# Kernel tuning notes

Hardware: AMD Instinct MI355X
Metric: run time of the kernel (lower is better)

## Reference

```python
import jax, jax.numpy as jnp
import numpy as np


def _fps_one_batch(pts, num_samples):
    """Furthest point sampling for one batch segment.
    pts: [Npb, 3]. Seeds with point 0 (pointops furthestsampling convention).
    Returns int32 indices [num_samples].
    """
    # initial min-distance to the seed point
    dist = jnp.sum((pts - pts[0]) ** 2, axis=-1)  # [Npb]

    def step(dist, _):
        idx = jnp.argmax(dist)                      # furthest remaining point
        d = jnp.sum((pts - pts[idx]) ** 2, axis=-1)  # dist to new sample
        return jnp.minimum(dist, d), idx.astype(jnp.int32)

    _, idxs = jax.lax.scan(step, dist, None, length=num_samples - 1)
    return jnp.concatenate([jnp.zeros((1,), jnp.int32), idxs])


def setup_inputs() -> dict:
    key = jax.random.key(0)
    N, B = 262144, 2
    Npb = N // B
    xyz = jax.random.normal(key, (N, 3), dtype=jnp.float32) * 20.0  # lidar-scale coords
    b = jnp.repeat(jnp.arange(B, dtype=jnp.float32), Npb)[:, None]
    point_bxyz = jnp.concatenate([b, xyz], axis=1)  # [N, 4] (b, x, y, z)
    return {"point_bxyz": point_bxyz, "stride": 32, "batch_size": B}


def reference(point_bxyz, stride, batch_size):
    N = point_bxyz.shape[0]
    Npb = N // batch_size                      # equal-size batch segments
    M = (Npb + stride - 1) // stride           # samples per batch (ceil)
    xyz = point_bxyz[:, 1:4].reshape(batch_size, Npb, 3)

    idx = jax.vmap(lambda p: _fps_one_batch(p, M))(xyz)          # [B, M] local indices
    gidx = idx + (jnp.arange(batch_size, dtype=jnp.int32) * Npb)[:, None]
    new_bxyz = point_bxyz[gidx.reshape(-1)]    # [B*M, 4] sampled points
    return new_bxyz
```

## Files before the change

kernel.cpp:

```cpp
#include <hip/hip_runtime.h>


#define NB    32
#define TPB   256
#define PPT   16
#define NPB   131072
#define MSAMP 4096
#define RING  2
#define KW    8
#define NWAVE 128
#define NQUAD (NWAVE * 16)
#define RB_U32 (NQUAD * 4)
#define NCAND (NWAVE * KW)
#define JCAP  64

typedef unsigned long long u64;
typedef unsigned int u32;
typedef __attribute__((ext_vector_type(4))) u32 u32x4;

__device__ __forceinline__ void st16_sys(u32* p, u32x4 v) {
  asm volatile("global_store_dwordx4 %0, %1, off sc0 sc1"
               :: "v"(p), "v"(v) : "memory");
}
__device__ __forceinline__ void ld16x8_sys(
    const u32* p0, const u32* p1, const u32* p2, const u32* p3,
    const u32* p4, const u32* p5, const u32* p6, const u32* p7,
    u32x4& q0, u32x4& q1, u32x4& q2, u32x4& q3,
    u32x4& q4, u32x4& q5, u32x4& q6, u32x4& q7) {
  asm volatile(
    "global_load_dwordx4 %0, %8, off sc0 sc1\n\t"
    "global_load_dwordx4 %1, %9, off sc0 sc1\n\t"
    "global_load_dwordx4 %2, %10, off sc0 sc1\n\t"
    "global_load_dwordx4 %3, %11, off sc0 sc1\n\t"
    "global_load_dwordx4 %4, %12, off sc0 sc1\n\t"
    "global_load_dwordx4 %5, %13, off sc0 sc1\n\t"
    "global_load_dwordx4 %6, %14, off sc0 sc1\n\t"
    "global_load_dwordx4 %7, %15, off sc0 sc1\n\t"
    "s_waitcnt vmcnt(0)"
    : "=v"(q0), "=v"(q1), "=v"(q2), "=v"(q3),
      "=v"(q4), "=v"(q5), "=v"(q6), "=v"(q7)
    : "v"(p0), "v"(p1), "v"(p2), "v"(p3),
      "v"(p4), "v"(p5), "v"(p6), "v"(p7)
    : "memory");
}

template<int CTRL>
__device__ __forceinline__ u64 dpp_move64(u64 x) {
  int lo = (int)(u32)(x & 0xFFFFFFFFull);
  int hi = (int)(u32)(x >> 32);
  int nlo = __builtin_amdgcn_update_dpp(lo, lo, CTRL, 0xF, 0xF, false);
  int nhi = __builtin_amdgcn_update_dpp(hi, hi, CTRL, 0xF, 0xF, false);
  return ((u64)(u32)nhi << 32) | (u64)(u32)nlo;
}
#define DPP_ROW_SHR(n)  (0x110 + (n))
#define DPP_BCAST15     0x142
#define DPP_BCAST31     0x143

__device__ __forceinline__ u64 dpp_max64_to63(u64 k) {
  u64 t;
  t = dpp_move64<DPP_ROW_SHR(1)>(k); if (t > k) k = t;
  t = dpp_move64<DPP_ROW_SHR(2)>(k); if (t > k) k = t;
  t = dpp_move64<DPP_ROW_SHR(4)>(k); if (t > k) k = t;
  t = dpp_move64<DPP_ROW_SHR(8)>(k); if (t > k) k = t;
  t = dpp_move64<DPP_BCAST15>(k);    if (t > k) k = t;
  t = dpp_move64<DPP_BCAST31>(k);    if (t > k) k = t;
  return k;
}
__device__ __forceinline__ u64 bcast_key(u64 k, int srclane) {
  u32 lo = (u32)__builtin_amdgcn_readlane((int)(u32)(k & 0xFFFFFFFFull), srclane);
  u32 hi = (u32)__builtin_amdgcn_readlane((int)(u32)(k >> 32), srclane);
  return ((u64)hi << 32) | (u64)lo;
}
__device__ __forceinline__ float bcast_f32(float v, int srclane) {
  return __uint_as_float((u32)__builtin_amdgcn_readlane((int)__float_as_uint(v), srclane));
}

template<int NC>
__device__ __forceinline__ int sim_wave(const u32* s_pool, int m, u32 cutd,
    int jmax, int lane, float& ox, float& oy, float& oz) {
#pragma clang fp contract(off)
  u64 ck[NC]; float cx[NC], cy[NC], cz[NC];
#pragma unroll
  for (int i = 0; i < NC; ++i) {
    int idx = lane + i * 64;
    if (idx < m) {
      const u32* b = s_pool + idx * 5;
      ck[i] = ((u64)b[1] << 32) | (u64)b[0];
      cx[i] = __uint_as_float(b[2]); cy[i] = __uint_as_float(b[3]);
      cz[i] = __uint_as_float(b[4]);
    } else { ck[i] = 0; cx[i] = cy[i] = cz[i] = 0.f; }
  }
  int j = 0;
  for (int t = 0; t < jmax; ++t) {
    u64 tk = ck[0]; float mx = cx[0], my = cy[0], mz = cz[0];
#pragma unroll
    for (int i = 1; i < NC; ++i)
      if (ck[i] > tk) { tk = ck[i]; mx = cx[i]; my = cy[i]; mz = cz[i]; }
    u64 wk = bcast_key(dpp_max64_to63(tk), 63);
    if (t > 0 && (u32)(wk >> 32) <= cutd) break;
    int wl = __ffsll(__ballot(tk == wk)) - 1;
    float wx = bcast_f32(mx, wl), wy = bcast_f32(my, wl), wz = bcast_f32(mz, wl);
    if (lane == t) { ox = wx; oy = wy; oz = wz; }
    j = t + 1;
#pragma unroll
    for (int i = 0; i < NC; ++i) {
      float dx = cx[i]-wx, dy = cy[i]-wy, dz = cz[i]-wz;
      float d2 = __fadd_rn(__fadd_rn(__fmul_rn(dx,dx), __fmul_rn(dy,dy)),
                           __fmul_rn(dz,dz));
      float nd = fminf(__uint_as_float((u32)(ck[i] >> 32)), d2);
      ck[i] = ((u64)__float_as_uint(nd) << 32) | (ck[i] & 0xFFFFFFFFull);
    }
  }
  return j;
}

__global__ __launch_bounds__(TPB, 1)
void fps_kernel(const float4* __restrict__ pts, float* __restrict__ out,
                u32* __restrict__ slots)
{
#pragma clang fp contract(off)
  const int batch = blockIdx.x >> 5;
  const int rank  = blockIdx.x & (NB - 1);
  const int tid   = threadIdx.x;
  const int lane  = tid & 63;
  const int wv    = tid >> 6;
  const int ws_id = rank * 4 + wv;

  __shared__ u32   s_quads[NWAVE * 68];
  __shared__ u32   s_pool[NCAND * 5];
  __shared__ int   s_cnt2[2];

  const float4* bpts = pts + (size_t)batch * NPB;
  u32* bslots = slots + (size_t)batch * (RING * RB_U32);
  const int base = rank * (TPB * PPT);

  float px[PPT], py[PPT], pz[PPT], dist[PPT];
  float4 seed = bpts[0];
  const float sx = seed.y, sy = seed.z, sz = seed.w;
#pragma unroll
  for (int k = 0; k < PPT; ++k) {
    float4 p = bpts[base + k * TPB + tid];
    px[k] = p.y; py[k] = p.z; pz[k] = p.w;
    float dx = px[k]-sx, dy = py[k]-sy, dz = pz[k]-sz;
    dist[k] = __fadd_rn(__fadd_rn(__fmul_rn(dx,dx), __fmul_rn(dy,dy)),
                        __fmul_rn(dz,dz));
  }
  if (rank == 0 && tid == 0) {
    float4 o; o.x=(float)batch; o.y=sx; o.z=sy; o.w=sz;
    *(float4*)(out + (size_t)batch * MSAMP * 4) = o;
  }
  if (tid == 0) { s_cnt2[0] = 0; s_cnt2[1] = 0; }
  __syncthreads();

  int S = 0; u32 r = 0;
  float ox = 0.f, oy = 0.f, oz = 0.f;

  while (S < MSAMP - 1) {
    r += 1;
    const int rem = (MSAMP - 1) - S;
    const int jmax = (rem < JCAP) ? rem : JCAP;

    u32 mask = 0; u64 tk = 0; float tx=0.f, ty=0.f, tz=0.f; int tbk = 0;
#pragma unroll
    for (int k = 0; k < PPT; ++k) {
      u64 kk = ((u64)__float_as_uint(dist[k]) << 32) | ((u64)r << 17) |
               (u64)(0x1FFFF - (base + k * TPB + tid));
      if (kk > tk) { tk = kk; tx = px[k]; ty = py[k]; tz = pz[k]; tbk = k; }
    }
    u32x4 shipq;
    for (int c = 0; c < KW; ++c) {
      u64 wk = bcast_key(dpp_max64_to63(tk), 63);
      int wl = __ffsll(__ballot(tk == wk)) - 1;
      float wx = bcast_f32(tx, wl), wy = bcast_f32(ty, wl), wz = bcast_f32(tz, wl);
      if (lane == 2*c)     { shipq.x=(u32)(wk & 0xFFFFFFFFull); shipq.y=(u32)(wk>>32);
                             shipq.z=__float_as_uint(wx); shipq.w=__float_as_uint(wy); }
      if (lane == 2*c + 1) { shipq.x=r; shipq.y=__float_as_uint(wz);
                             shipq.z=0u; shipq.w=0u; }
      if (tk == wk) {
        mask |= 1u << tbk;
        tk = 0; tx = ty = tz = 0.f; tbk = 0;
#pragma unroll
        for (int k = 0; k < PPT; ++k) {
          if (!((mask >> k) & 1u)) {
            u64 kk = ((u64)__float_as_uint(dist[k]) << 32) | ((u64)r << 17) |
                     (u64)(0x1FFFF - (base + k * TPB + tid));
            if (kk > tk) { tk = kk; tx = px[k]; ty = py[k]; tz = pz[k]; tbk = k; }
          }
        }
      }
    }

    u32* ring = bslots + (size_t)(r & (RING - 1)) * RB_U32;
    if (lane < 16) st16_sys(ring + (ws_id * 16 + lane) * 4, shipq);

    const int gb = wv * 512 + lane;
    const u32 *pp0 = ring + (gb      ) * 4, *pp1 = ring + (gb +  64) * 4,
              *pp2 = ring + (gb + 128) * 4, *pp3 = ring + (gb + 192) * 4,
              *pp4 = ring + (gb + 256) * 4, *pp5 = ring + (gb + 320) * 4,
              *pp6 = ring + (gb + 384) * 4, *pp7 = ring + (gb + 448) * 4;
    u32x4 q0,q1,q2,q3,q4,q5,q6,q7;
    for (u32 it = 0; ; ++it) {
      ld16x8_sys(pp0,pp1,pp2,pp3,pp4,pp5,pp6,pp7, q0,q1,q2,q3,q4,q5,q6,q7);
      bool ok;
      if ((lane & 1) == 0)
        ok = ((q0.x>>17)==r)&&((q1.x>>17)==r)&&((q2.x>>17)==r)&&((q3.x>>17)==r)&&
             ((q4.x>>17)==r)&&((q5.x>>17)==r)&&((q6.x>>17)==r)&&((q7.x>>17)==r);
      else
        ok = (q0.x==r)&&(q1.x==r)&&(q2.x==r)&&(q3.x==r)&&
             (q4.x==r)&&(q5.x==r)&&(q6.x==r)&&(q7.x==r);
      if (__ballot(ok) == ~0ull) break;
      __builtin_amdgcn_s_sleep(1);
    }
    if (tid == 0) s_cnt2[(r + 1) & 1] = 0;
    {
      int g = gb;
      *(u32x4*)&s_quads[(g>>4)*68 + (g&15)*4] = q0; g += 64;
      *(u32x4*)&s_quads[(g>>4)*68 + (g&15)*4] = q1; g += 64;
      *(u32x4*)&s_quads[(g>>4)*68 + (g&15)*4] = q2; g += 64;
      *(u32x4*)&s_quads[(g>>4)*68 + (g&15)*4] = q3; g += 64;
      *(u32x4*)&s_quads[(g>>4)*68 + (g&15)*4] = q4; g += 64;
      *(u32x4*)&s_quads[(g>>4)*68 + (g&15)*4] = q5; g += 64;
      *(u32x4*)&s_quads[(g>>4)*68 + (g&15)*4] = q6; g += 64;
      *(u32x4*)&s_quads[(g>>4)*68 + (g&15)*4] = q7;
    }
    __syncthreads();

    u64 cutk;
    {
      int w0 = lane, w1 = lane + 64;
      u64 k0 = ((u64)s_quads[w0*68 + 57] << 32) | (u64)s_quads[w0*68 + 56];
      u64 k1 = ((u64)s_quads[w1*68 + 57] << 32) | (u64)s_quads[w1*68 + 56];
      u64 ct = (k0 > k1) ? k0 : k1;
      cutk = bcast_key(dpp_max64_to63(ct), 63);
    }
    const u32 cutd = (u32)(cutk >> 32);

    int* cnt = &s_cnt2[r & 1];
    bool hh[4]; int myoff[4]; int tot = 0;
    u32 clo[4], chi[4], cx4[4], cy4[4], cz4[4];
    const u64 ltmask = (1ull << lane) - 1ull;
#pragma unroll
    for (int i = 0; i < 4; ++i) {
      int cg = tid * 4 + i;
      int qb = (cg >> 3) * 68 + (cg & 7) * 8;
      u32 lo = s_quads[qb], hi = s_quads[qb + 1];
      u64 kk = ((u64)hi << 32) | (u64)lo;
      clo[i] = lo; chi[i] = hi;
      cx4[i] = s_quads[qb+2]; cy4[i] = s_quads[qb+3]; cz4[i] = s_quads[qb+5];
      hh[i] = kk > cutk;
      u64 b = __ballot(hh[i]);
      myoff[i] = tot + __popcll(b & ltmask);
      tot += __popcll(b);
    }
    int pbase = 0;
    if (lane == 0) pbase = atomicAdd(cnt, tot);
    pbase = __builtin_amdgcn_readfirstlane(pbase);
#pragma unroll
    for (int i = 0; i < 4; ++i)
      if (hh[i]) {
        u32* d = &s_pool[(pbase + myoff[i]) * 5];
        d[0]=clo[i]; d[1]=chi[i]; d[2]=cx4[i]; d[3]=cy4[i]; d[4]=cz4[i];
      }
    __syncthreads();
    const int m = *cnt;

    int j;
    if      (m <=  64) j = sim_wave<1>(s_pool, m, cutd, jmax, lane, ox, oy, oz);
    else if (m <= 128) j = sim_wave<2>(s_pool, m, cutd, jmax, lane, ox, oy, oz);
    else if (m <= 256) j = sim_wave<4>(s_pool, m, cutd, jmax, lane, ox, oy, oz);
    else if (m <= 512) j = sim_wave<8>(s_pool, m, cutd, jmax, lane, ox, oy, oz);
    else               j = sim_wave<14>(s_pool, m, cutd, jmax, lane, ox, oy, oz);

    if (rank == 0 && wv == 0 && lane < j) {
      float4 o; o.x = (float)batch; o.y = ox; o.z = oy; o.w = oz;
      *(float4*)(out + (size_t)(batch * MSAMP + S + 1 + lane) * 4) = o;
    }
    for (int i = 0; i < j; ++i) {
      float wx = bcast_f32(ox, i), wy = bcast_f32(oy, i), wz = bcast_f32(oz, i);
#pragma unroll
      for (int k = 0; k < PPT; ++k) {
        float dx = px[k]-wx, dy = py[k]-wy, dz = pz[k]-wz;
        float d2 = __fadd_rn(__fadd_rn(__fmul_rn(dx,dx), __fmul_rn(dy,dy)),
                             __fmul_rn(dz,dz));
        dist[k] = fminf(dist[k], d2);
      }
    }
    S += j;
  }
}

extern "C" void kernel_launch(void* const* d_in, const int* in_sizes, int n_in,
                              void* d_out, int out_size, void* d_ws, size_t ws_size,
                              hipStream_t stream) {
  const float4* pts = (const float4*)d_in[0];
  float* out = (float*)d_out;
  u32* slots = (u32*)d_ws;

  hipMemsetAsync(d_ws, 0, (size_t)2 * RING * RB_U32 * 4, stream);

  dim3 grid(2 * NB), block(TPB);
  hipLaunchKernelGGL(fps_kernel, grid, block, 0, stream, pts, out, slots);
}
```

Before: 3.613 ms.

## Ship 16 candidates per wave and compact pool via index list

Each wave now publishes 16 top candidates per round instead of 8, so every round exchanges a larger candidate set and can resolve more samples per global synchronisation. The exchange buffer is read with 16 system-coherent loads into a mirror array in shared memory. Pool compaction now writes 16-bit indices into that array instead of copying candidate records. The cost is more cross-block traffic per round, wider register arrays, and larger per-wave simulation loops (up to 30 candidates per lane).

```diff
diff --git a/kernel.cpp b/kernel.cpp
--- a/kernel.cpp
+++ b/kernel.cpp
@@ -7,40 +7,50 @@
 #define NPB   131072
 #define MSAMP 4096
 #define RING  2
-#define KW    8
+#define KW    16
 #define NWAVE 128
-#define NQUAD (NWAVE * 16)
+#define NQUAD (NWAVE * 32)
 #define RB_U32 (NQUAD * 4)
 #define NCAND (NWAVE * KW)
 #define JCAP  64
 
 typedef unsigned long long u64;
 typedef unsigned int u32;
+typedef unsigned short u16;
 typedef __attribute__((ext_vector_type(4))) u32 u32x4;
 
 __device__ __forceinline__ void st16_sys(u32* p, u32x4 v) {
   asm volatile("global_store_dwordx4 %0, %1, off sc0 sc1"
                :: "v"(p), "v"(v) : "memory");
 }
-__device__ __forceinline__ void ld16x8_sys(
-    const u32* p0, const u32* p1, const u32* p2, const u32* p3,
-    const u32* p4, const u32* p5, const u32* p6, const u32* p7,
-    u32x4& q0, u32x4& q1, u32x4& q2, u32x4& q3,
-    u32x4& q4, u32x4& q5, u32x4& q6, u32x4& q7) {
+__device__ __forceinline__ void ld16x16_sys(
+    const u32* const* p, u32x4* q) {
   asm volatile(
-    "global_load_dwordx4 %0, %8, off sc0 sc1\n\t"
-    "global_load_dwordx4 %1, %9, off sc0 sc1\n\t"
-    "global_load_dwordx4 %2, %10, off sc0 sc1\n\t"
-    "global_load_dwordx4 %3, %11, off sc0 sc1\n\t"
-    "global_load_dwordx4 %4, %12, off sc0 sc1\n\t"
-    "global_load_dwordx4 %5, %13, off sc0 sc1\n\t"
-    "global_load_dwordx4 %6, %14, off sc0 sc1\n\t"
-    "global_load_dwordx4 %7, %15, off sc0 sc1\n\t"
+    "global_load_dwordx4 %0, %16, off sc0 sc1\n\t"
+    "global_load_dwordx4 %1, %17, off sc0 sc1\n\t"
+    "global_load_dwordx4 %2, %18, off sc0 sc1\n\t"
+    "global_load_dwordx4 %3, %19, off sc0 sc1\n\t"
+    "global_load_dwordx4 %4, %20, off sc0 sc1\n\t"
+    "global_load_dwordx4 %5, %21, off sc0 sc1\n\t"
+    "global_load_dwordx4 %6, %22, off sc0 sc1\n\t"
+    "global_load_dwordx4 %7, %23, off sc0 sc1\n\t"
+    "global_load_dwordx4 %8, %24, off sc0 sc1\n\t"
+    "global_load_dwordx4 %9, %25, off sc0 sc1\n\t"
+    "global_load_dwordx4 %10, %26, off sc0 sc1\n\t"
+    "global_load_dwordx4 %11, %27, off sc0 sc1\n\t"
+    "global_load_dwordx4 %12, %28, off sc0 sc1\n\t"
+    "global_load_dwordx4 %13, %29, off sc0 sc1\n\t"
+    "global_load_dwordx4 %14, %30, off sc0 sc1\n\t"
+    "global_load_dwordx4 %15, %31, off sc0 sc1\n\t"
     "s_waitcnt vmcnt(0)"
-    : "=v"(q0), "=v"(q1), "=v"(q2), "=v"(q3),
-      "=v"(q4), "=v"(q5), "=v"(q6), "=v"(q7)
-    : "v"(p0), "v"(p1), "v"(p2), "v"(p3),
-      "v"(p4), "v"(p5), "v"(p6), "v"(p7)
+    : "=v"(q[0]), "=v"(q[1]), "=v"(q[2]), "=v"(q[3]),
+      "=v"(q[4]), "=v"(q[5]), "=v"(q[6]), "=v"(q[7]),
+      "=v"(q[8]), "=v"(q[9]), "=v"(q[10]), "=v"(q[11]),
+      "=v"(q[12]), "=v"(q[13]), "=v"(q[14]), "=v"(q[15])
+    : "v"(p[0]), "v"(p[1]), "v"(p[2]), "v"(p[3]),
+      "v"(p[4]), "v"(p[5]), "v"(p[6]), "v"(p[7]),
+      "v"(p[8]), "v"(p[9]), "v"(p[10]), "v"(p[11]),
+      "v"(p[12]), "v"(p[13]), "v"(p[14]), "v"(p[15])
     : "memory");
 }
 
@@ -76,15 +86,15 @@
 }
 
 template<int NC>
-__device__ __forceinline__ int sim_wave(const u32* s_pool, int m, u32 cutd,
-    int jmax, int lane, float& ox, float& oy, float& oz) {
+__device__ __forceinline__ int sim_wave(const u32* s_mir, const u16* s_pidx,
+    int m, u32 cutd, int jmax, int lane, float& ox, float& oy, float& oz) {
 #pragma clang fp contract(off)
   u64 ck[NC]; float cx[NC], cy[NC], cz[NC];
 #pragma unroll
   for (int i = 0; i < NC; ++i) {
     int idx = lane + i * 64;
     if (idx < m) {
-      const u32* b = s_pool + idx * 5;
+      const u32* b = s_mir + (int)s_pidx[idx] * 5;
       ck[i] = ((u64)b[1] << 32) | (u64)b[0];
       cx[i] = __uint_as_float(b[2]); cy[i] = __uint_as_float(b[3]);
       cz[i] = __uint_as_float(b[4]);
@@ -126,8 +136,8 @@
   const int wv    = tid >> 6;
   const int ws_id = rank * 4 + wv;
 
-  __shared__ u32   s_quads[NWAVE * 68];
-  __shared__ u32   s_pool[NCAND * 5];
+  __shared__ u32   s_mir[NCAND * 5];
+  __shared__ u16   s_pidx[NCAND];
   __shared__ int   s_cnt2[2];
 
   const float4* bpts = pts + (size_t)batch * NPB;
@@ -191,62 +201,57 @@
     }
 
     u32* ring = bslots + (size_t)(r & (RING - 1)) * RB_U32;
-    if (lane < 16) st16_sys(ring + (ws_id * 16 + lane) * 4, shipq);
-
-    const int gb = wv * 512 + lane;
-    const u32 *pp0 = ring + (gb      ) * 4, *pp1 = ring + (gb +  64) * 4,
-              *pp2 = ring + (gb + 128) * 4, *pp3 = ring + (gb + 192) * 4,
-              *pp4 = ring + (gb + 256) * 4, *pp5 = ring + (gb + 320) * 4,
-              *pp6 = ring + (gb + 384) * 4, *pp7 = ring + (gb + 448) * 4;
-    u32x4 q0,q1,q2,q3,q4,q5,q6,q7;
-    for (u32 it = 0; ; ++it) {
-      ld16x8_sys(pp0,pp1,pp2,pp3,pp4,pp5,pp6,pp7, q0,q1,q2,q3,q4,q5,q6,q7);
+    if (lane < 32)
+      st16_sys(ring + ((ws_id * 16 + (lane >> 1)) * 8 + (lane & 1) * 4), shipq);
+
+    const int gb = wv * 1024 + lane;
+    const u32* pp[16]; u32x4 q[16];
+#pragma unroll
+    for (int i = 0; i < 16; ++i) pp[i] = ring + (size_t)(gb + 64 * i) * 4;
+    for (;;) {
+      ld16x16_sys(pp, q);
       bool ok;
-      if ((lane & 1) == 0)
-        ok = ((q0.x>>17)==r)&&((q1.x>>17)==r)&&((q2.x>>17)==r)&&((q3.x>>17)==r)&&
-             ((q4.x>>17)==r)&&((q5.x>>17)==r)&&((q6.x>>17)==r)&&((q7.x>>17)==r);
-      else
-        ok = (q0.x==r)&&(q1.x==r)&&(q2.x==r)&&(q3.x==r)&&
-             (q4.x==r)&&(q5.x==r)&&(q6.x==r)&&(q7.x==r);
+      if ((lane & 1) == 0) {
+        ok = true;
+#pragma unroll
+        for (int i = 0; i < 16; ++i) ok = ok && ((q[i].x >> 17) == r);
+      } else {
+        ok = true;
+#pragma unroll
+        for (int i = 0; i < 16; ++i) ok = ok && (q[i].x == r);
+      }
       if (__ballot(ok) == ~0ull) break;
       __builtin_amdgcn_s_sleep(1);
     }
     if (tid == 0) s_cnt2[(r + 1) & 1] = 0;
     {
-      int g = gb;
-      *(u32x4*)&s_quads[(g>>4)*68 + (g&15)*4] = q0; g += 64;
-      *(u32x4*)&s_quads[(g>>4)*68 + (g&15)*4] = q1; g += 64;
-      *(u32x4*)&s_quads[(g>>4)*68 + (g&15)*4] = q2; g += 64;
-      *(u32x4*)&s_quads[(g>>4)*68 + (g&15)*4] = q3; g += 64;
-      *(u32x4*)&s_quads[(g>>4)*68 + (g&15)*4] = q4; g += 64;
-      *(u32x4*)&s_quads[(g>>4)*68 + (g&15)*4] = q5; g += 64;
-      *(u32x4*)&s_quads[(g>>4)*68 + (g&15)*4] = q6; g += 64;
-      *(u32x4*)&s_quads[(g>>4)*68 + (g&15)*4] = q7;
+#pragma unroll
+      for (int i = 0; i < 16; ++i) {
+        int C = (gb + 64 * i) >> 1;
+        u32* d = &s_mir[C * 5];
+        if ((lane & 1) == 0) { d[0]=q[i].x; d[1]=q[i].y; d[2]=q[i].z; d[3]=q[i].w; }
+        else                 { d[4]=q[i].y; }
+      }
     }
     __syncthreads();
 
     u64 cutk;
     {
-      int w0 = lane, w1 = lane + 64;
-      u64 k0 = ((u64)s_quads[w0*68 + 57] << 32) | (u64)s_quads[w0*68 + 56];
-      u64 k1 = ((u64)s_quads[w1*68 + 57] << 32) | (u64)s_quads[w1*68 + 56];
+      int c0 = lane * 16 + 15, c1 = (lane + 64) * 16 + 15;
+      u64 k0 = ((u64)s_mir[c0*5 + 1] << 32) | (u64)s_mir[c0*5];
+      u64 k1 = ((u64)s_mir[c1*5 + 1] << 32) | (u64)s_mir[c1*5];
       u64 ct = (k0 > k1) ? k0 : k1;
       cutk = bcast_key(dpp_max64_to63(ct), 63);
     }
     const u32 cutd = (u32)(cutk >> 32);
 
     int* cnt = &s_cnt2[r & 1];
-    bool hh[4]; int myoff[4]; int tot = 0;
-    u32 clo[4], chi[4], cx4[4], cy4[4], cz4[4];
+    bool hh[8]; int myoff[8]; int tot = 0;
     const u64 ltmask = (1ull << lane) - 1ull;
 #pragma unroll
-    for (int i = 0; i < 4; ++i) {
-      int cg = tid * 4 + i;
-      int qb = (cg >> 3) * 68 + (cg & 7) * 8;
-      u32 lo = s_quads[qb], hi = s_quads[qb + 1];
-      u64 kk = ((u64)hi << 32) | (u64)lo;
-      clo[i] = lo; chi[i] = hi;
-      cx4[i] = s_quads[qb+2]; cy4[i] = s_quads[qb+3]; cz4[i] = s_quads[qb+5];
+    for (int i = 0; i < 8; ++i) {
+      int cg = tid * 8 + i;
+      u64 kk = ((u64)s_mir[cg*5 + 1] << 32) | (u64)s_mir[cg*5];
       hh[i] = kk > cutk;
       u64 b = __ballot(hh[i]);
       myoff[i] = tot + __popcll(b & ltmask);
@@ -256,20 +261,16 @@
     if (lane == 0) pbase = atomicAdd(cnt, tot);
     pbase = __builtin_amdgcn_readfirstlane(pbase);
 #pragma unroll
-    for (int i = 0; i < 4; ++i)
-      if (hh[i]) {
-        u32* d = &s_pool[(pbase + myoff[i]) * 5];
-        d[0]=clo[i]; d[1]=chi[i]; d[2]=cx4[i]; d[3]=cy4[i]; d[4]=cz4[i];
-      }
+    for (int i = 0; i < 8; ++i)
+      if (hh[i]) s_pidx[pbase + myoff[i]] = (u16)(tid * 8 + i);
     __syncthreads();
     const int m = *cnt;
 
     int j;
-    if      (m <=  64) j = sim_wave<1>(s_pool, m, cutd, jmax, lane, ox, oy, oz);
-    else if (m <= 128) j = sim_wave<2>(s_pool, m, cutd, jmax, lane, ox, oy, oz);
-    else if (m <= 256) j = sim_wave<4>(s_pool, m, cutd, jmax, lane, ox, oy, oz);
-    else if (m <= 512) j = sim_wave<8>(s_pool, m, cutd, jmax, lane, ox, oy, oz);
-    else               j = sim_wave<14>(s_pool, m, cutd, jmax, lane, ox, oy, oz);
+    if      (m <= 512)  j = sim_wave<8> (s_mir, s_pidx, m, cutd, jmax, lane, ox, oy, oz);
+    else if (m <= 896)  j = sim_wave<14>(s_mir, s_pidx, m, cutd, jmax, lane, ox, oy, oz);
+    else if (m <= 1408) j = sim_wave<22>(s_mir, s_pidx, m, cutd, jmax, lane, ox, oy, oz);
+    else                j = sim_wave<30>(s_mir, s_pidx, m, cutd, jmax, lane, ox, oy, oz);
 
     if (rank == 0 && wv == 0 && lane < j) {
       float4 o; o.x = (float)batch; o.y = ox; o.z = oy; o.w = oz;
```

Result: slower. 6.014 ms (+66.4%).
